# Kernel tuning notes

Measured on AMD Instinct MI355X. Metric: run time of the kernel, lower is better.

## Reference

```python
import jax, jax.numpy as jnp
import numpy as np

NUM_CLASSES = 128


def setup_inputs() -> dict:
    key = jax.random.key(0)
    k1, k2, k3 = jax.random.split(key, 3)
    B, T, C = 64, 2048, NUM_CLASSES
    emissions = jax.random.normal(k1, (B, T, C), dtype=jnp.float32)
    tags = jax.random.randint(k2, (B, T), 0, C, dtype=jnp.int32)
    # learned params (glorot-ish scale for transitions, zeros for start/end)
    transitions = jax.random.normal(k3, (C, C), dtype=jnp.float32) * 0.1
    start_transitions = jnp.zeros((C,), dtype=jnp.float32)
    end_transitions = jnp.zeros((C,), dtype=jnp.float32)
    return {
        "emissions": emissions,
        "tags": tags,
        "transitions": transitions,
        "start_transitions": start_transitions,
        "end_transitions": end_transitions,
    }


def _log_partition(emissions, trans, start, end):
    # forward algorithm: sequential logsumexp-add semiring scan over T
    alpha0 = start + emissions[:, 0]                      # (B, C)
    em_rest = jnp.swapaxes(emissions[:, 1:], 0, 1)        # (T-1, B, C)

    def step(alpha, emit):
        scores = alpha[:, :, None] + trans[None]          # (B, C_from, C_to)
        alpha = jax.nn.logsumexp(scores, axis=1) + emit   # (B, C)
        return alpha, None

    alpha, _ = jax.lax.scan(step, alpha0, em_rest)
    return jax.nn.logsumexp(alpha + end, axis=-1)         # (B,)


def _gold_score(emissions, tags, trans, start, end):
    emit_total = jnp.take_along_axis(emissions, tags[:, :, None], axis=2)[:, :, 0].sum(-1)  # (B,)
    trans_total = trans[tags[:, :-1], tags[:, 1:]].sum(-1)                                  # (B,)
    return start[tags[:, 0]] + emit_total + trans_total + end[tags[:, -1]]


def _viterbi(emissions, trans, start, end):
    v0 = start + emissions[:, 0]                          # (B, C)
    em_rest = jnp.swapaxes(emissions[:, 1:], 0, 1)        # (T-1, B, C)

    def step(v, emit):
        scores = v[:, :, None] + trans[None]              # (B, C_from, C_to)
        best_from = jnp.argmax(scores, axis=1).astype(jnp.int32)  # (B, C)
        v = jnp.max(scores, axis=1) + emit
        return v, best_from

    v, bps = jax.lax.scan(step, v0, em_rest)              # bps: (T-1, B, C)
    v = v + end
    best_last = jnp.argmax(v, axis=-1).astype(jnp.int32)  # (B,)

    def back(best, bp):
        best = jnp.take_along_axis(bp, best[:, None], axis=1)[:, 0]
        return best, best

    _, path_rev = jax.lax.scan(back, best_last, bps, reverse=True)  # (T-1, B)
    paths = jnp.concatenate([path_rev, best_last[None]], axis=0)    # (T, B)
    return paths.T                                                   # (B, T)


def reference(emissions, tags, transitions, start_transitions, end_transitions):
    trans, start, end = transitions, start_transitions, end_transitions
    # CRF NLL (training loss path): log Z - gold path score
    log_Z = _log_partition(emissions, trans, start, end)
    gold = _gold_score(emissions, tags, trans, start, end)
    nll = log_Z - gold                                    # (B,)
    # inference path: one-hot Viterbi decode, as in call(training=False)
    paths = _viterbi(emissions, trans, start, end)        # (B, T)
    onehot = jax.nn.one_hot(paths, NUM_CLASSES, dtype=emissions.dtype)  # (B, T, C)
    return nll, onehot
```

## Files before the change

### kernel.cpp

```cpp
#include <hip/hip_runtime.h>
#include <stdint.h>

#define NB 64
#define NT 2048
#define NC 128
#define KF 32
#define LF 64
#define WF 16
#define NVB 128
#define KV 8
#define LV 256
#define WV 64

typedef _Float16 h2 __attribute__((ext_vector_type(2)));

__device__ __forceinline__ h2 bc2(uint32_t u) { return __builtin_bit_cast(h2, u); }

__device__ __forceinline__ float fdot2f(h2 a, h2 b, float c) {
#if __has_builtin(__builtin_amdgcn_fdot2)
  return __builtin_amdgcn_fdot2(a, b, c, false);
#else
  float d;
  asm("v_dot2_f32_f16 %0, %1, %2, %3"
      : "=v"(d)
      : "v"(__builtin_bit_cast(uint32_t, a)), "v"(__builtin_bit_cast(uint32_t, b)), "v"(c));
  return d;
#endif
}

#define DPP_FMAX_STAGE(vv, ctrl)                                               \
  {                                                                            \
    int t_ = __builtin_amdgcn_update_dpp(vv, vv, ctrl, 0xf, 0xf, false);       \
    vv = __builtin_bit_cast(int, fmaxf(__builtin_bit_cast(float, vv),          \
                                       __builtin_bit_cast(float, t_)));        \
  }

__device__ __forceinline__ float wave_max_bcast(float x) {
  int v = __builtin_bit_cast(int, x);
  DPP_FMAX_STAGE(v, 0x111);
  DPP_FMAX_STAGE(v, 0x112);
  DPP_FMAX_STAGE(v, 0x114);
  DPP_FMAX_STAGE(v, 0x118);
  DPP_FMAX_STAGE(v, 0x142);
  DPP_FMAX_STAGE(v, 0x143);
  return __builtin_bit_cast(float, __builtin_amdgcn_readlane(v, 63));
}

__device__ __forceinline__ float readlanef(float v, int l) {
  return __builtin_bit_cast(float, __builtin_amdgcn_readlane(__builtin_bit_cast(int, v), l));
}

__device__ __forceinline__ int mbcnt64(unsigned long long m) {
  return __builtin_amdgcn_mbcnt_hi((uint32_t)(m >> 32),
                                   __builtin_amdgcn_mbcnt_lo((uint32_t)m, 0));
}

__device__ __forceinline__ size_t slot_off(int b, int t) {
  return ((size_t)64 + ((size_t)b * NT + t) * NC) * 4;
}

union ScanSM {
  float itr[64 * 256];
  uint32_t ea[4][2][64];
};

__global__ __launch_bounds__(256, 1) void scan_kernel(
    const float* __restrict__ em, const float* __restrict__ trans,
    const float* __restrict__ startv, const float* __restrict__ endv,
    float* __restrict__ out, float* __restrict__ fpart, int* __restrict__ best_last) {
  __shared__ __align__(16) ScanSM sm;
  const int lane = threadIdx.x & 63;
  const int wid = threadIdx.x >> 6;

  if (blockIdx.x >= NVB) {
    const int fi = (blockIdx.x - NVB) * 4 + wid;
    const int b = fi >> 5, c = fi & 31;
    const int t0 = (c == 0) ? 0 : c * LF - WF;
    const int tend = (c == KF - 1) ? (NT - 1) : (c + 1) * LF;
    const float* emb = em + (size_t)b * NT * NC;

    h2 e0[64], e1[64];
#pragma unroll
    for (int j = 0; j < 64; ++j) {
      float2 r0 = *(const float2*)(trans + (size_t)(2 * j) * NC + 2 * lane);
      float2 r1 = *(const float2*)(trans + (size_t)(2 * j + 1) * NC + 2 * lane);
      h2 a, bb;
      a.x = (_Float16)__expf(r0.x);  a.y = (_Float16)__expf(r1.x);
      bb.x = (_Float16)__expf(r0.y); bb.y = (_Float16)__expf(r1.y);
      e0[j] = a; e1[j] = bb;
    }
    float2 ev = *(const float2*)(endv + 2 * lane);
    float2 em0 = *(const float2*)(emb + (size_t)t0 * NC + 2 * lane);
    float2 nx0 = *(const float2*)(emb + (size_t)(t0 + 1) * NC + 2 * lane);
    float2 nx1 = *(const float2*)(emb + (size_t)(t0 + 2) * NC + 2 * lane);
    float2 nx2 = *(const float2*)(emb + (size_t)(t0 + 3) * NC + 2 * lane);
    float2 nx3 = *(const float2*)(emb + (size_t)(t0 + 4) * NC + 2 * lane);
    float u0 = em0.x, u1 = em0.y;
    if (c == 0) {
      float2 sv = *(const float2*)(startv + 2 * lane);
      u0 += sv.x; u1 += sv.y;
    }
    float mu = 0.f;
    uint32_t* eab0 = &sm.ea[wid][0][0];
    uint32_t* eab1 = &sm.ea[wid][1][0];

    auto fstep = [&](int t, float2& nx) {
      h2 eh; eh.x = (_Float16)__expf(u0); eh.y = (_Float16)__expf(u1);
      uint32_t* eab = (t & 1) ? eab1 : eab0;
      eab[lane] = __builtin_bit_cast(uint32_t, eh);
      float nm = wave_max_bcast(fmaxf(u0, u1));
      asm volatile("s_waitcnt lgkmcnt(0)" ::: "memory");
      float A0 = 0.f, A1 = 0.f, A2 = 0.f, A3 = 0.f;
#pragma unroll
      for (int q = 0; q < 16; ++q) {
        uint4 w = *(const uint4*)&eab[q * 4];
        A0 = fdot2f(bc2(w.x), e0[4 * q + 0], A0); A1 = fdot2f(bc2(w.x), e1[4 * q + 0], A1);
        A2 = fdot2f(bc2(w.y), e0[4 * q + 1], A2); A3 = fdot2f(bc2(w.y), e1[4 * q + 1], A3);
        A0 = fdot2f(bc2(w.z), e0[4 * q + 2], A0); A1 = fdot2f(bc2(w.z), e1[4 * q + 2], A1);
        A2 = fdot2f(bc2(w.w), e0[4 * q + 3], A2); A3 = fdot2f(bc2(w.w), e1[4 * q + 3], A3);
      }
      float o0 = nx.x - nm, o1 = nx.y - nm;
      u0 = __logf(A0 + A2) + o0;
      u1 = __logf(A1 + A3) + o1;
      mu += nm;
      if (t + 4 <= tend) nx = *(const float2*)(emb + (size_t)(t + 4) * NC + 2 * lane);
    };

    auto wave_lse = [&](float x0, float x1) -> float {
      float m = wave_max_bcast(fmaxf(x0, x1));
      float ss = __expf(x0 - m) + __expf(x1 - m);
#pragma unroll
      for (int s = 1; s < 64; s <<= 1) ss += __shfl_xor(ss, s, 64);
      return m + __logf(ss);
    };

    int t = t0 + 1;
    float m_start = 0.f;
    if (c > 0) {
      for (int j = 0; j < WF / 4; ++j) {
        fstep(t, nx0); fstep(t + 1, nx1); fstep(t + 2, nx2); fstep(t + 3, nx3);
        t += 4;
      }
      m_start = mu + wave_lse(u0, u1);
    }
    for (; t + 3 <= tend; t += 4) {
      fstep(t, nx0); fstep(t + 1, nx1); fstep(t + 2, nx2); fstep(t + 3, nx3);
    }
    int rem = tend - t + 1;
    if (rem > 0) fstep(t, nx0);
    if (rem > 1) fstep(t + 1, nx1);
    if (rem > 2) fstep(t + 2, nx2);

    float m_end;
    if (c == KF - 1) m_end = mu + wave_lse(u0 + ev.x, u1 + ev.y);
    else             m_end = mu + wave_lse(u0, u1);
    if (lane == 0) fpart[b * KF + c] = m_end - m_start;
  } else {
    const int fi = blockIdx.x * 4 + wid;
    const int b = fi >> 3, c = fi & 7;
    const float* emb = em + (size_t)b * NT * NC;
    char* ob = (char*)out;
    for (int r = wid * 32; r < wid * 32 + 32; ++r) {
      float2 w = *(const float2*)(trans + (size_t)r * NC + 2 * lane);
      int l = r >> 1, p = r & 1;
      sm.itr[l * 256 + (2 * lane) * 2 + p] = w.x;
      sm.itr[l * 256 + (2 * lane + 1) * 2 + p] = w.y;
    }
    __syncthreads();
    float rmx0 = -INFINITY, rmn0 = INFINITY, rmx1 = -INFINITY, rmn1 = INFINITY;
    for (int j = 0; j < 64; ++j) {
      int jj = (j + lane) & 63;
      float4 q = *(const float4*)&sm.itr[lane * 256 + jj * 4];
      rmx0 = fmaxf(rmx0, fmaxf(q.x, q.z)); rmn0 = fminf(rmn0, fminf(q.x, q.z));
      rmx1 = fmaxf(rmx1, fmaxf(q.y, q.w)); rmn1 = fminf(rmn1, fminf(q.y, q.w));
    }

    const int trec = c * LV;
    const int tend = trec + LV;
    float2 ev = *(const float2*)(endv + 2 * lane);
    float v0, v1;
    int t;
    if (c == 0) {
      float2 sv = *(const float2*)(startv + 2 * lane);
      float2 em0 = *(const float2*)(emb + 2 * lane);
      v0 = sv.x + em0.x; v1 = sv.y + em0.y;
      t = 1;
    } else {
      int t0 = trec - 1 - WV;
      float2 em0 = *(const float2*)(emb + (size_t)t0 * NC + 2 * lane);
      v0 = em0.x; v1 = em0.y;
      t = t0 + 1;
    }
    float2 nx0 = *(const float2*)(emb + (size_t)t * NC + 2 * lane);
    float2 nx1 = *(const float2*)(emb + (size_t)(t + 1) * NC + 2 * lane);
    float2 nx2 = *(const float2*)(emb + (size_t)(t + 2) * NC + 2 * lane);
    float2 nx3 = *(const float2*)(emb + (size_t)(t + 3) * NC + 2 * lane);
    const float4* itb = (const float4*)&sm.itr[4 * lane];

    auto cmax = [&](int l, float4 q, float& c0, float& c1) {
      float ve = readlanef(v0, l);
      float vo = readlanef(v1, l);
      c0 = fmaxf(ve + q.x, vo + q.y);
      c1 = fmaxf(ve + q.z, vo + q.w);
    };

    auto wstep = [&](int tt, float2& nx) {
      float thr = wave_max_bcast(fmaxf(v0 + rmn0, v1 + rmn1));
      unsigned long long m0 = __ballot(v0 + rmx0 >= thr);
      unsigned long long m1 = __ballot(v1 + rmx1 >= thr);
      unsigned long long r = m0 | m1;
      if (!r) r = 1ull;
      int cnt = (int)__popcll(r);
      float best0, best1;
      if (__builtin_expect(cnt <= 4, 1)) {
        int l0 = (int)__builtin_ctzll(r); r &= r - 1;
        int l1 = r ? (int)__builtin_ctzll(r) : l0; r = r ? (r & (r - 1)) : 0ull;
        int l2 = r ? (int)__builtin_ctzll(r) : l0; r = r ? (r & (r - 1)) : 0ull;
        int l3 = r ? (int)__builtin_ctzll(r) : l0; r = r ? (r & (r - 1)) : 0ull;
        float4 q0 = itb[l0 * 64], q1 = itb[l1 * 64], q2 = itb[l2 * 64], q3 = itb[l3 * 64];
        float a0, a1, b0c, b1c, c0c, c1c, d0c, d1c;
        cmax(l0, q0, a0, a1); cmax(l1, q1, b0c, b1c);
        cmax(l2, q2, c0c, c1c); cmax(l3, q3, d0c, d1c);
        best0 = fmaxf(fmaxf(a0, b0c), fmaxf(c0c, d0c));
        best1 = fmaxf(fmaxf(a1, b1c), fmaxf(c1c, d1c));
      } else {
        int l0 = (int)__builtin_ctzll(r); r &= r - 1;
        int l1 = r ? (int)__builtin_ctzll(r) : l0; r = r ? (r & (r - 1)) : 0ull;
        int l2 = r ? (int)__builtin_ctzll(r) : l0; r = r ? (r & (r - 1)) : 0ull;
        int l3 = r ? (int)__builtin_ctzll(r) : l0; r = r ? (r & (r - 1)) : 0ull;
        float4 q0 = itb[l0 * 64], q1 = itb[l1 * 64], q2 = itb[l2 * 64], q3 = itb[l3 * 64];
        float a0, a1, b0c, b1c, c0c, c1c, d0c, d1c;
        cmax(l0, q0, a0, a1); cmax(l1, q1, b0c, b1c);
        cmax(l2, q2, c0c, c1c); cmax(l3, q3, d0c, d1c);
        best0 = fmaxf(fmaxf(a0, b0c), fmaxf(c0c, d0c));
        best1 = fmaxf(fmaxf(a1, b1c), fmaxf(c1c, d1c));
        while (r) {
          int la = (int)__builtin_ctzll(r); r &= r - 1;
          int lb = r ? (int)__builtin_ctzll(r) : la; r = r ? (r & (r - 1)) : 0ull;
          int lc = r ? (int)__builtin_ctzll(r) : la; r = r ? (r & (r - 1)) : 0ull;
          int ld = r ? (int)__builtin_ctzll(r) : la; r = r ? (r & (r - 1)) : 0ull;
          float4 qa = itb[la * 64], qb = itb[lb * 64], qc = itb[lc * 64], qd = itb[ld * 64];
          float x0, x1, y0, y1, z0, z1, w0, w1;
          cmax(la, qa, x0, x1); cmax(lb, qb, y0, y1);
          cmax(lc, qc, z0, z1); cmax(ld, qd, w0, w1);
          best0 = fmaxf(best0, fmaxf(fmaxf(x0, y0), fmaxf(z0, w0)));
          best1 = fmaxf(best1, fmaxf(fmaxf(x1, y1), fmaxf(z1, w1)));
        }
      }
      v0 = best0 + nx.x; v1 = best1 + nx.y;
      if (tt + 4 < NT) nx = *(const float2*)(emb + (size_t)(tt + 4) * NC + 2 * lane);
    };

    auto vstep = [&](int tt, float2& nx) {
      float thr = wave_max_bcast(fmaxf(v0 + rmn0, v1 + rmn1));
      unsigned long long m0 = __ballot(v0 + rmx0 >= thr);
      unsigned long long m1 = __ballot(v1 + rmx1 >= thr);
      unsigned long long rem = m0 | m1;
      if (!rem) rem = 1ull;
      int cnt = (int)__popcll(rem);
      int nvals = (int)__popcll(m0) + (int)__popcll(m1);
      char* rec = ob + slot_off(b, tt);
      float best0, best1;

      if (__builtin_expect(nvals <= 92, 1)) {
        if (lane == 0) {
          *(unsigned long long*)(rec + 128) = m0;
          *(unsigned long long*)(rec + 136) = m1;
        }
        int plt = mbcnt64(m0) + mbcnt64(m1);
        int hasE = (int)((m0 >> lane) & 1ull);
        if (hasE) *(float*)(rec + 144 + 4 * plt) = v0;
        if ((m1 >> lane) & 1ull) *(float*)(rec + 144 + 4 * (plt + hasE)) = v1;
        unsigned long long r = rem;
        if (__builtin_expect(cnt <= 4, 1)) {
          int l0 = (int)__builtin_ctzll(r); r &= r - 1;
          int l1 = r ? (int)__builtin_ctzll(r) : l0; r = r ? (r & (r - 1)) : 0ull;
          int l2 = r ? (int)__builtin_ctzll(r) : l0; r = r ? (r & (r - 1)) : 0ull;
          int l3 = r ? (int)__builtin_ctzll(r) : l0; r = r ? (r & (r - 1)) : 0ull;
          float4 q0 = itb[l0 * 64], q1 = itb[l1 * 64], q2 = itb[l2 * 64], q3 = itb[l3 * 64];
          float a0, a1, b0c, b1c, c0c, c1c, d0c, d1c;
          cmax(l0, q0, a0, a1); cmax(l1, q1, b0c, b1c);
          cmax(l2, q2, c0c, c1c); cmax(l3, q3, d0c, d1c);
          best0 = fmaxf(fmaxf(a0, b0c), fmaxf(c0c, d0c));
          best1 = fmaxf(fmaxf(a1, b1c), fmaxf(c1c, d1c));
        } else {
          int l0 = (int)__builtin_ctzll(r); r &= r - 1;
          int l1 = r ? (int)__builtin_ctzll(r) : l0; r = r ? (r & (r - 1)) : 0ull;
          int l2 = r ? (int)__builtin_ctzll(r) : l0; r = r ? (r & (r - 1)) : 0ull;
          int l3 = r ? (int)__builtin_ctzll(r) : l0; r = r ? (r & (r - 1)) : 0ull;
          int l4 = r ? (int)__builtin_ctzll(r) : l0; r = r ? (r & (r - 1)) : 0ull;
          int l5 = r ? (int)__builtin_ctzll(r) : l0; r = r ? (r & (r - 1)) : 0ull;
          int l6 = r ? (int)__builtin_ctzll(r) : l0; r = r ? (r & (r - 1)) : 0ull;
          int l7 = r ? (int)__builtin_ctzll(r) : l0; r = r ? (r & (r - 1)) : 0ull;
          float4 q0 = itb[l0 * 64], q1 = itb[l1 * 64], q2 = itb[l2 * 64], q3 = itb[l3 * 64];
          float4 q4 = itb[l4 * 64], q5 = itb[l5 * 64], q6 = itb[l6 * 64], q7 = itb[l7 * 64];
          float a0, a1, b0c, b1c, c0c, c1c, d0c, d1c;
          float e0c, e1c, f0c, f1c, g0c, g1c, h0c, h1c;
          cmax(l0, q0, a0, a1); cmax(l1, q1, b0c, b1c);
          cmax(l2, q2, c0c, c1c); cmax(l3, q3, d0c, d1c);
          cmax(l4, q4, e0c, e1c); cmax(l5, q5, f0c, f1c);
          cmax(l6, q6, g0c, g1c); cmax(l7, q7, h0c, h1c);
          best0 = fmaxf(fmaxf(fmaxf(a0, b0c), fmaxf(c0c, d0c)),
                        fmaxf(fmaxf(e0c, f0c), fmaxf(g0c, h0c)));
          best1 = fmaxf(fmaxf(fmaxf(a1, b1c), fmaxf(c1c, d1c)),
                        fmaxf(fmaxf(e1c, f1c), fmaxf(g1c, h1c)));
          while (r) {
            int la = (int)__builtin_ctzll(r); r &= r - 1;
            int lb = r ? (int)__builtin_ctzll(r) : la; r = r ? (r & (r - 1)) : 0ull;
            int lc = r ? (int)__builtin_ctzll(r) : la; r = r ? (r & (r - 1)) : 0ull;
            int ld = r ? (int)__builtin_ctzll(r) : la; r = r ? (r & (r - 1)) : 0ull;
            float4 qa = itb[la * 64], qb = itb[lb * 64], qc = itb[lc * 64], qd = itb[ld * 64];
            float x0, x1, y0, y1, z0, z1, w0, w1;
            cmax(la, qa, x0, x1); cmax(lb, qb, y0, y1);
            cmax(lc, qc, z0, z1); cmax(ld, qd, w0, w1);
            best0 = fmaxf(best0, fmaxf(fmaxf(x0, y0), fmaxf(z0, w0)));
            best1 = fmaxf(best1, fmaxf(fmaxf(x1, y1), fmaxf(z1, w1)));
          }
        }
      } else {
        if (lane == 0) {
          *(unsigned long long*)(rec + 128) = 0ull;
          *(unsigned long long*)(rec + 136) = 0ull;
        }
        best0 = -INFINITY; best1 = -INFINITY;
        int bi0 = 0, bi1 = 0;
        unsigned long long r = rem;
        do {
          int l0 = (int)__builtin_ctzll(r); r &= r - 1;
          int l1 = l0, l2 = l0, l3 = l0;
          if (r) {
            l1 = (int)__builtin_ctzll(r); r &= r - 1;
            if (r) {
              l2 = (int)__builtin_ctzll(r); r &= r - 1;
              if (r) { l3 = (int)__builtin_ctzll(r); r &= r - 1; }
            }
          }
          float4 q0 = itb[l0 * 64], q1 = itb[l1 * 64], q2 = itb[l2 * 64], q3 = itb[l3 * 64];
          auto proc = [&](int lc, float4 q) {
            if ((m0 >> lc) & 1ull) {
              float vce = readlanef(v0, lc);
              float s0 = vce + q.x, s1 = vce + q.z;
              bool g0 = s0 > best0; best0 = g0 ? s0 : best0; bi0 = g0 ? 2 * lc : bi0;
              bool g1 = s1 > best1; best1 = g1 ? s1 : best1; bi1 = g1 ? 2 * lc : bi1;
            }
            if ((m1 >> lc) & 1ull) {
              float vco = readlanef(v1, lc);
              float s0 = vco + q.y, s1 = vco + q.w;
              bool g0 = s0 > best0; best0 = g0 ? s0 : best0; bi0 = g0 ? 2 * lc + 1 : bi0;
              bool g1 = s1 > best1; best1 = g1 ? s1 : best1; bi1 = g1 ? 2 * lc + 1 : bi1;
            }
          };
          proc(l0, q0); proc(l1, q1); proc(l2, q2); proc(l3, q3);
        } while (r);
        *(uint16_t*)(rec + 2 * lane) = (uint16_t)((bi0 & 0xff) | (bi1 << 8));
      }

      v0 = best0 + nx.x; v1 = best1 + nx.y;
      if (tt + 4 < NT) nx = *(const float2*)(emb + (size_t)(tt + 4) * NC + 2 * lane);
    };

    if (c > 0) {
      for (int k = 0; k < WV / 4; ++k) {
        wstep(t, nx0); wstep(t + 1, nx1); wstep(t + 2, nx2); wstep(t + 3, nx3);
        t += 4;
      }
    }
    for (; t + 3 < tend; t += 4) {
      vstep(t, nx0); vstep(t + 1, nx1); vstep(t + 2, nx2); vstep(t + 3, nx3);
    }
    if (t < tend) vstep(t, nx0);
    if (t + 1 < tend) vstep(t + 1, nx1);
    if (t + 2 < tend) vstep(t + 2, nx2);

    if (c == KV - 1) {
      v0 += ev.x; v1 += ev.y;
      float bv = v0; int bix = 2 * lane;
      if (v1 > bv) { bv = v1; bix = 2 * lane + 1; }
#pragma unroll
      for (int s = 1; s < 64; s <<= 1) {
        float ovv = __shfl_xor(bv, s, 64);
        int oi = __shfl_xor(bix, s, 64);
        if (ovv > bv || (ovv == bv && oi < bix)) { bv = ovv; bix = oi; }
      }
      if (lane == 0) best_last[b] = bix;
    }
  }
}

__global__ __launch_bounds__(128) void bpgold_kernel(
    const float* __restrict__ em, const int* __restrict__ tags,
    const float* __restrict__ trans, const float* __restrict__ startv,
    const float* __restrict__ endv, float* __restrict__ out,
    float* __restrict__ gold) {
  __shared__ float red[128];
  if (blockIdx.x >= 2048) {
    int b = blockIdx.x - 2048, tid = threadIdx.x;
    const float* emb = em + (size_t)b * NT * NC;
    const int* tgb = tags + (size_t)b * NT;
    float acc = 0.f;
    for (int j = 0; j < NT / 128; ++j) {
      int t = tid + j * 128;
      int tg = tgb[t];
      acc += emb[(size_t)t * NC + tg];
      if (t < NT - 1) acc += trans[(size_t)tg * NC + tgb[t + 1]];
    }
    red[tid] = acc;
    __syncthreads();
    for (int s = 64; s > 0; s >>= 1) {
      if (tid < s) red[tid] += red[tid + s];
      __syncthreads();
    }
    if (tid == 0) gold[b] = red[0] + startv[tgb[0]] + endv[tgb[NT - 1]];
    return;
  }
  int bid = blockIdx.x, b = bid >> 5, cc = bid & 31, ct = threadIdx.x;
  char* ob = (char*)out;
  int lo = cc * 64, hi = cc * 64 + 63;
  if (lo < 1) lo = 1;
  for (int t = lo; t <= hi; ++t) {
    char* rec = ob + slot_off(b, t);
    unsigned long long m0 = *(const unsigned long long*)(rec + 128);
    unsigned long long m1 = *(const unsigned long long*)(rec + 136);
    unsigned long long rem = m0 | m1;
    if (rem == 0ull) continue;
    const float* vals = (const float*)(rec + 144);
    float best = -INFINITY;
    int bi = 0, idx = 0;
    do {
      int l = (int)__builtin_ctzll(rem); rem &= rem - 1;
      if ((m0 >> l) & 1ull) {
        float s = vals[idx++] + trans[(size_t)(2 * l) * NC + ct];
        if (s > best) { best = s; bi = 2 * l; }
      }
      if ((m1 >> l) & 1ull) {
        float s = vals[idx++] + trans[(size_t)(2 * l + 1) * NC + ct];
        if (s > best) { best = s; bi = 2 * l + 1; }
      }
    } while (rem);
    ((uint8_t*)rec)[ct] = (uint8_t)bi;
  }
}

__global__ __launch_bounds__(128) void maps_kernel(const float* __restrict__ out,
                                                   uint8_t* __restrict__ mmap) {
  __shared__ uint8_t bp[256 * 128];
  int bid = blockIdx.x, b = bid >> 3, c = bid & 7, tid = threadIdx.x;
  const char* ob = (const char*)out;
  int lo_t = c * 256 + 1;
  int nrows = (c == 7) ? 255 : 256;
  int nd = nrows * 32;
  for (int k = 0; k < 64; ++k) {
    int d = tid + k * 128;
    if (d < nd) {
      int row = d >> 5, col = d & 31;
      *(uint32_t*)&bp[(size_t)d * 4] =
          *(const uint32_t*)(ob + slot_off(b, lo_t + row) + (size_t)col * 4);
    }
  }
  __syncthreads();
  int cur = tid;
  for (int i = nrows - 1; i >= 0; --i) cur = bp[i * 128 + cur];
  mmap[b * 1024 + c * 128 + tid] = (uint8_t)cur;
}

__global__ void boundary_kernel(const uint8_t* __restrict__ mmap,
                                const int* __restrict__ best_last,
                                const float* __restrict__ fpart,
                                const float* __restrict__ gold,
                                uint8_t* __restrict__ TOPa,
                                float* __restrict__ out) {
  int b = threadIdx.x;
  const uint8_t* ob = (const uint8_t*)out;
  int e = best_last[b];
  for (int c = 7; c >= 0; --c) {
    TOPa[b * 8 + c] = (c == 7) ? (uint8_t)e : ob[slot_off(b, 256 * (c + 1)) + e];
    e = mmap[b * 1024 + c * 128 + e];
  }
  float z = 0.f;
  for (int c = 0; c < KF; ++c) z += fpart[b * KF + c];
  out[b] = z - gold[b];
}

__global__ __launch_bounds__(128) void replay_kernel(float* __restrict__ out,
                                                     const uint8_t* __restrict__ TOPa) {
  __shared__ uint8_t bp[255 * 128];
  __shared__ uint8_t path[256];
  int bid = blockIdx.x, b = bid >> 3, c = bid & 7, tid = threadIdx.x;
  char* ob = (char*)out;
  int lo_t = c * 256 + 1;
  const int nd = 255 * 32;
  for (int k = 0; k < 64; ++k) {
    int d = tid + k * 128;
    if (d < nd) {
      int row = d >> 5, col = d & 31;
      *(uint32_t*)&bp[(size_t)d * 4] =
          *(const uint32_t*)(ob + slot_off(b, lo_t + row) + (size_t)col * 4);
    }
  }
  __syncthreads();
  if (tid == 0) {
    int cur = TOPa[b * 8 + c];
    path[255] = (uint8_t)cur;
    for (int i = 254; i >= 0; --i) { cur = bp[i * 128 + cur]; path[i] = (uint8_t)cur; }
  }
  __syncthreads();
  for (int k = 0; k < 64; ++k) {
    int idx = tid + k * 128;
    int row = idx >> 5, j = idx & 31;
    int p = path[row];
    int c0 = j * 4;
    float4 val;
    val.x = (c0 + 0 == p) ? 1.f : 0.f;
    val.y = (c0 + 1 == p) ? 1.f : 0.f;
    val.z = (c0 + 2 == p) ? 1.f : 0.f;
    val.w = (c0 + 3 == p) ? 1.f : 0.f;
    *(float4*)(ob + slot_off(b, c * 256 + row) + (size_t)j * 16) = val;
  }
}

extern "C" void kernel_launch(void* const* d_in, const int* in_sizes, int n_in,
                              void* d_out, int out_size, void* d_ws, size_t ws_size,
                              hipStream_t stream) {
  const float* em = (const float*)d_in[0];
  const int* tags = (const int*)d_in[1];
  const float* trans = (const float*)d_in[2];
  const float* startv = (const float*)d_in[3];
  const float* endv = (const float*)d_in[4];
  float* out = (float*)d_out;
  char* ws = (char*)d_ws;
  float* fpart = (float*)(ws + 0);
  float* gold = (float*)(ws + 8192);
  int* best_last = (int*)(ws + 8448);
  uint8_t* TOPa = (uint8_t*)(ws + 8704);
  uint8_t* mmap = (uint8_t*)(ws + 9216);

  scan_kernel<<<dim3(NVB + 512), dim3(256), 0, stream>>>(em, trans, startv, endv, out,
                                                         fpart, best_last);
  bpgold_kernel<<<dim3(2048 + 64), dim3(128), 0, stream>>>(em, tags, trans, startv,
                                                           endv, out, gold);
  maps_kernel<<<dim3(512), dim3(128), 0, stream>>>(out, mmap);
  boundary_kernel<<<dim3(1), dim3(64), 0, stream>>>(mmap, best_last, fpart, gold, TOPa, out);
  replay_kernel<<<dim3(512), dim3(128), 0, stream>>>(out, TOPa);
}
```

Measured before the change: 369.4 us.

## Split Viterbi scan into more chunks and remove the single-thread boundary kernel

Doubles the number of Viterbi time chunks (16 chunks of 128 steps per batch row, 256 blocks) so more waves run the sequential max-plus scan in parallel over shorter spans. It drops the single-block boundary kernel: NLL finalization moves into the gold-score blocks, and each replay block walks the chunk maps itself, with a new tmap holding each chunk's last backpointer row. It also removes the duplicate fast-path branch in the warmup step. The risk is inconsistency, because the maps and replay kernels still assume 8 chunks of 256 steps while the scan now uses 16 of 128, and more warmup work is redundant.

```diff
diff --git a/kernel.cpp b/kernel.cpp
--- a/kernel.cpp
+++ b/kernel.cpp
@@ -7,9 +7,9 @@
 #define KF 32
 #define LF 64
 #define WF 16
-#define NVB 128
-#define KV 8
-#define LV 256
+#define NVB 256
+#define KV 16
+#define LV 128
 #define WV 64
 
 typedef _Float16 h2 __attribute__((ext_vector_type(2)));
@@ -157,7 +157,7 @@
     if (lane == 0) fpart[b * KF + c] = m_end - m_start;
   } else {
     const int fi = blockIdx.x * 4 + wid;
-    const int b = fi >> 3, c = fi & 7;
+    const int b = fi >> 4, c = fi & 15;
     const float* emb = em + (size_t)b * NT * NC;
     char* ob = (char*)out;
     for (int r = wid * 32; r < wid * 32 + 32; ++r) {
@@ -212,18 +212,7 @@
       if (!r) r = 1ull;
       int cnt = (int)__popcll(r);
       float best0, best1;
-      if (__builtin_expect(cnt <= 4, 1)) {
-        int l0 = (int)__builtin_ctzll(r); r &= r - 1;
-        int l1 = r ? (int)__builtin_ctzll(r) : l0; r = r ? (r & (r - 1)) : 0ull;
-        int l2 = r ? (int)__builtin_ctzll(r) : l0; r = r ? (r & (r - 1)) : 0ull;
-        int l3 = r ? (int)__builtin_ctzll(r) : l0; r = r ? (r & (r - 1)) : 0ull;
-        float4 q0 = itb[l0 * 64], q1 = itb[l1 * 64], q2 = itb[l2 * 64], q3 = itb[l3 * 64];
-        float a0, a1, b0c, b1c, c0c, c1c, d0c, d1c;
-        cmax(l0, q0, a0, a1); cmax(l1, q1, b0c, b1c);
-        cmax(l2, q2, c0c, c1c); cmax(l3, q3, d0c, d1c);
-        best0 = fmaxf(fmaxf(a0, b0c), fmaxf(c0c, d0c));
-        best1 = fmaxf(fmaxf(a1, b1c), fmaxf(c1c, d1c));
-      } else {
+      {
         int l0 = (int)__builtin_ctzll(r); r &= r - 1;
         int l1 = r ? (int)__builtin_ctzll(r) : l0; r = r ? (r & (r - 1)) : 0ull;
         int l2 = r ? (int)__builtin_ctzll(r) : l0; r = r ? (r & (r - 1)) : 0ull;
@@ -247,6 +236,7 @@
           best1 = fmaxf(best1, fmaxf(fmaxf(x1, y1), fmaxf(z1, w1)));
         }
       }
+      (void)cnt;
       v0 = best0 + nx.x; v1 = best1 + nx.y;
       if (tt + 4 < NT) nx = *(const float2*)(emb + (size_t)(tt + 4) * NC + 2 * lane);
     };
@@ -391,7 +381,7 @@
     const float* __restrict__ em, const int* __restrict__ tags,
     const float* __restrict__ trans, const float* __restrict__ startv,
     const float* __restrict__ endv, float* __restrict__ out,
-    float* __restrict__ gold) {
+    const float* __restrict__ fpart) {
   __shared__ float red[128];
   if (blockIdx.x >= 2048) {
     int b = blockIdx.x - 2048, tid = threadIdx.x;
@@ -410,7 +400,11 @@
       if (tid < s) red[tid] += red[tid + s];
       __syncthreads();
     }
-    if (tid == 0) gold[b] = red[0] + startv[tgb[0]] + endv[tgb[NT - 1]];
+    if (tid == 0) {
+      float z = 0.f;
+      for (int c = 0; c < KF; ++c) z += fpart[b * KF + c];
+      out[b] = z - (red[0] + startv[tgb[0]] + endv[tgb[NT - 1]]);
+    }
     return;
   }
   int bid = blockIdx.x, b = bid >> 5, cc = bid & 31, ct = threadIdx.x;
@@ -442,7 +436,8 @@
 }
 
 __global__ __launch_bounds__(128) void maps_kernel(const float* __restrict__ out,
-                                                   uint8_t* __restrict__ mmap) {
+                                                   uint8_t* __restrict__ mmap,
+                                                   uint8_t* __restrict__ tmap) {
   __shared__ uint8_t bp[256 * 128];
   int bid = blockIdx.x, b = bid >> 3, c = bid & 7, tid = threadIdx.x;
   const char* ob = (const char*)out;
@@ -461,28 +456,13 @@
   int cur = tid;
   for (int i = nrows - 1; i >= 0; --i) cur = bp[i * 128 + cur];
   mmap[b * 1024 + c * 128 + tid] = (uint8_t)cur;
-}
-
-__global__ void boundary_kernel(const uint8_t* __restrict__ mmap,
-                                const int* __restrict__ best_last,
-                                const float* __restrict__ fpart,
-                                const float* __restrict__ gold,
-                                uint8_t* __restrict__ TOPa,
-                                float* __restrict__ out) {
-  int b = threadIdx.x;
-  const uint8_t* ob = (const uint8_t*)out;
-  int e = best_last[b];
-  for (int c = 7; c >= 0; --c) {
-    TOPa[b * 8 + c] = (c == 7) ? (uint8_t)e : ob[slot_off(b, 256 * (c + 1)) + e];
-    e = mmap[b * 1024 + c * 128 + e];
-  }
-  float z = 0.f;
-  for (int c = 0; c < KF; ++c) z += fpart[b * KF + c];
-  out[b] = z - gold[b];
+  if (c < 7) tmap[b * 1024 + c * 128 + tid] = bp[255 * 128 + tid];
 }
 
 __global__ __launch_bounds__(128) void replay_kernel(float* __restrict__ out,
-                                                     const uint8_t* __restrict__ TOPa) {
+                                                     const uint8_t* __restrict__ mmap,
+                                                     const uint8_t* __restrict__ tmap,
+                                                     const int* __restrict__ best_last) {
   __shared__ uint8_t bp[255 * 128];
   __shared__ uint8_t path[256];
   int bid = blockIdx.x, b = bid >> 3, c = bid & 7, tid = threadIdx.x;
@@ -499,7 +479,9 @@
   }
   __syncthreads();
   if (tid == 0) {
-    int cur = TOPa[b * 8 + c];
+    int e = best_last[b];
+    for (int cc = 7; cc > c; --cc) e = mmap[b * 1024 + cc * 128 + e];
+    int cur = (c == 7) ? best_last[b] : tmap[b * 1024 + c * 128 + e];
     path[255] = (uint8_t)cur;
     for (int i = 254; i >= 0; --i) { cur = bp[i * 128 + cur]; path[i] = (uint8_t)cur; }
   }
@@ -529,16 +511,14 @@
   float* out = (float*)d_out;
   char* ws = (char*)d_ws;
   float* fpart = (float*)(ws + 0);
-  float* gold = (float*)(ws + 8192);
-  int* best_last = (int*)(ws + 8448);
-  uint8_t* TOPa = (uint8_t*)(ws + 8704);
+  int* best_last = (int*)(ws + 8192);
   uint8_t* mmap = (uint8_t*)(ws + 9216);
+  uint8_t* tmap = (uint8_t*)(ws + 9216 + 65536);
 
   scan_kernel<<<dim3(NVB + 512), dim3(256), 0, stream>>>(em, trans, startv, endv, out,
                                                          fpart, best_last);
   bpgold_kernel<<<dim3(2048 + 64), dim3(128), 0, stream>>>(em, tags, trans, startv,
-                                                           endv, out, gold);
-  maps_kernel<<<dim3(512), dim3(128), 0, stream>>>(out, mmap);
-  boundary_kernel<<<dim3(1), dim3(64), 0, stream>>>(mmap, best_last, fpart, gold, TOPa, out);
-  replay_kernel<<<dim3(512), dim3(128), 0, stream>>>(out, TOPa);
-}
+                                                           endv, out, fpart);
+  maps_kernel<<<dim3(512), dim3(128), 0, stream>>>(out, mmap, tmap);
+  replay_kernel<<<dim3(512), dim3(128), 0, stream>>>(out, mmap, tmap, best_last);
+}
```

New measurement: 363.0 us. About the same (-1.7%).
